# Optimization experiments

Measured on AMD Instinct MI355X. Metric: run time of the kernel, lower is better.

The kernel has to match this reference:

```python
import jax, jax.numpy as jnp
import numpy as np

ALPHA = 32.0 ** 2
HEADS = 8
DIM_HEAD = 64
EPS = 1e-5


def _leaky(x):
    return jnp.where(x >= 0, x, 0.1 * x)


def _cpb_bias(fmap_size, w0, b0, w1, b1, w2, b2):
    # continuous position bias: MLP over signed-log relative coords -> [h, n, n]
    pos = jnp.arange(fmap_size)
    gi, gj = jnp.meshgrid(pos, pos, indexing='ij')
    grid = jnp.stack([gi, gj], axis=-1).reshape(-1, 2)  # [n, 2]
    rel = grid[:, None, :] - grid[None, :, :]           # [n, n, 2]
    rel = jnp.sign(rel) * jnp.log(jnp.abs(rel) + 1.0)
    h = _leaky(jnp.einsum('ijc,dc->ijd', rel.astype(jnp.float32), w0) + b0)
    h = _leaky(jnp.einsum('ijc,dc->ijd', h, w1) + b1)
    h = jnp.einsum('ijc,hc->ijh', h, w2) + b2           # [n, n, heads]
    return jnp.transpose(h, (2, 0, 1))                  # [heads, n, n]


def _stable_softmax(t, alpha=ALPHA):
    t = t / alpha
    t = t - jax.lax.stop_gradient(jnp.max(t, axis=-1, keepdims=True))
    return jax.nn.softmax(t * alpha, axis=-1)


def setup_inputs() -> dict:
    key = jax.random.key(0)
    ks = jax.random.split(key, 9)
    B, C, H, W = 8, 512, 32, 32
    inner = HEADS * DIM_HEAD
    s = 0.05
    return {
        'x': jax.random.normal(ks[0], (B, C, H, W), jnp.float32),
        'gamma': jnp.ones((1, C, 1, 1), jnp.float32),
        'w_qkv': jax.random.normal(ks[1], (inner * 3, C), jnp.float32) * s,
        'w_out': jax.random.normal(ks[2], (C, inner), jnp.float32) * s,
        'cpb_w0': jax.random.normal(ks[3], (128, 2), jnp.float32) * s,
        'cpb_b0': jax.random.normal(ks[4], (128,), jnp.float32) * s,
        'cpb_w1': jax.random.normal(ks[5], (128, 128), jnp.float32) * s,
        'cpb_b1': jax.random.normal(ks[6], (128,), jnp.float32) * s,
        'cpb_w2': jax.random.normal(ks[7], (HEADS, 128), jnp.float32) * s,
        'cpb_b2': jax.random.normal(ks[8], (HEADS,), jnp.float32) * s,
    }


def reference(x, gamma, w_qkv, w_out, cpb_w0, cpb_b0, cpb_w1, cpb_b1, cpb_w2, cpb_b2):
    B, C, H, W = x.shape
    n = H * W
    scale = DIM_HEAD ** -0.5
    residual = x

    # LayerNormChan: normalize over channel dim with biased variance
    mean = jnp.mean(x, axis=1, keepdims=True)
    var = jnp.var(x, axis=1, keepdims=True)
    xn = (x - mean) / jnp.sqrt(var + EPS) * gamma

    # 1x1 conv qkv projection as matmul over channels
    xf = xn.reshape(B, C, n)                              # [B, C, n]
    qkv = jnp.einsum('oc,bcn->bon', w_qkv, xf)            # [B, 3*inner, n]
    q, k, v = jnp.split(qkv, 3, axis=1)
    rs = lambda t: t.reshape(B, HEADS, DIM_HEAD, n)
    q, k, v = rs(q), rs(k), rs(v)

    sim = jnp.einsum('bhdi,bhdj->bhij', q, k) * scale     # [B, h, n, n]
    bias = _cpb_bias(H, cpb_w0, cpb_b0, cpb_w1, cpb_b1, cpb_w2, cpb_b2)
    sim = sim + bias[None]

    attn = _stable_softmax(sim)
    out = jnp.einsum('bhij,bhdj->bhdi', attn, v)          # [B, h, d, n]
    out = out.reshape(B, HEADS * DIM_HEAD, n)
    out = jnp.einsum('oc,bcn->bon', w_out, out).reshape(B, C, H, W)
    return out + residual
```

## Files before the change

kernel.cpp:

```cpp
#include <hip/hip_runtime.h>
#include <hip/hip_bf16.h>

#define CCH   512
#define BATCH 8
#define NPOS  1024
#define MQKV  1536
#define EPS   1e-5f
#define LOG2E 1.4426950408889634f

typedef __attribute__((ext_vector_type(4))) float f32x4;
typedef __attribute__((ext_vector_type(8))) __bf16 bf16x8;
typedef __attribute__((ext_vector_type(8))) unsigned short u16x8;
typedef __attribute__((ext_vector_type(4))) unsigned short u16x4;

__device__ inline unsigned short f2bf(float f) {
  __hip_bfloat16 h = __float2bfloat16(f);
  return __builtin_bit_cast(unsigned short, h);
}
__device__ inline float bf2f(unsigned short u) {
  return __bfloat162float(__builtin_bit_cast(__hip_bfloat16, u));
}

__device__ inline int sw(int row, int col) { return row * 64 + (col ^ ((row & 7) << 3)); }

__device__ inline void gload16(const void* g, void* l) {
  __builtin_amdgcn_global_load_lds((const __attribute__((address_space(1))) void*)g,
                                   (__attribute__((address_space(3))) void*)l, 16, 0, 0);
}

__global__ __launch_bounds__(256) void setup_kernel(
    const float* __restrict__ wq, const float* __restrict__ wo,
    unsigned short* __restrict__ wqb, unsigned short* __restrict__ wob,
    const float* __restrict__ x, const float* __restrict__ gamma,
    unsigned short* __restrict__ xnT) {
  __shared__ float red[4][32][2];
  __shared__ float gsh[512];
  __shared__ unsigned short obuf[32 * 520];
  int bid = blockIdx.x, tid = threadIdx.x;

  if (bid < 3072) {
    int i = bid * 256 + tid;
    if (i < MQKV * CCH) {
      float v = wq[i];
      if (i < 512 * CCH) v *= 0.125f * LOG2E;
      wqb[i] = f2bf(v);
    }
    if (i < CCH * CCH) wob[i] = f2bf(wo[i]);
  } else {
    int blk = bid - 3072;
    int b = blk >> 5, p0 = (blk & 31) * 32;
    int pl = tid & 31, wv = tid >> 6, cg = tid >> 5;
    gsh[tid] = gamma[tid];
    gsh[tid + 256] = gamma[tid + 256];
    const float* xp = x + (size_t)b * CCH * NPOS + p0 + pl;
    float vals[64];
    float s1 = 0.f, s2 = 0.f;
    #pragma unroll
    for (int j = 0; j < 64; ++j) {
      float v = xp[(size_t)(cg + 8 * j) * NPOS];
      vals[j] = v; s1 += v; s2 += v * v;
    }
    s1 += __shfl_xor(s1, 32, 64); s2 += __shfl_xor(s2, 32, 64);
    if ((tid & 63) < 32) { red[wv][pl][0] = s1; red[wv][pl][1] = s2; }
    __syncthreads();
    float t1 = 0.f, t2 = 0.f;
    #pragma unroll
    for (int w2i = 0; w2i < 4; ++w2i) { t1 += red[w2i][pl][0]; t2 += red[w2i][pl][1]; }
    float mean = t1 * (1.f / 512.f);
    float var = t2 * (1.f / 512.f) - mean * mean;
    float rstd = rsqrtf(var + EPS);
    #pragma unroll
    for (int j = 0; j < 64; ++j) {
      int c = cg + 8 * j;
      obuf[pl * 520 + c] = f2bf((vals[j] - mean) * rstd * gsh[c]);
    }
    __syncthreads();
    unsigned short* orow = xnT + ((size_t)b * NPOS + p0) * 512;
    #pragma unroll
    for (int i = 0; i < 8; ++i) {
      int c2 = tid + i * 256;
      int pp = c2 >> 6, ch = c2 & 63;
      *(u16x8*)&orow[(size_t)pp * 512 + ch * 8] = *(const u16x8*)&obuf[pp * 520 + ch * 8];
    }
  }
}

__global__ __launch_bounds__(256) void cpb_kernel(
    const float* __restrict__ w0, const float* __restrict__ b0,
    const float* __restrict__ w1, const float* __restrict__ b1,
    const float* __restrict__ w2, const float* __restrict__ b2,
    float* __restrict__ table) {
  __shared__ float w1s[128 * 129];
  __shared__ float w2s[8 * 128];
  __shared__ float sh1[2][128];
  __shared__ float sh2[2][128];
  int tid = threadIdx.x;
  #pragma unroll
  for (int i = 0; i < 64; ++i) {
    int idx = i * 256 + tid;
    w1s[(idx >> 7) * 129 + (idx & 127)] = w1[idx];
  }
  #pragma unroll
  for (int i = 0; i < 4; ++i) {
    int idx = i * 256 + tid;
    w2s[idx] = w2[idx];
  }
  int sub = tid >> 7, t = tid & 127;
  float w00 = w0[t * 2 + 0], w01 = w0[t * 2 + 1], bb0 = b0[t], bb1 = b1[t];
  int hh = t >> 4, k16 = t & 15;
  float b2h = b2[hh];
  __syncthreads();

  #pragma unroll 1
  for (int pass = 0; pass < 8; ++pass) {
    int d0 = (blockIdx.x * 8 + pass) * 2 + sub;
    bool ok = d0 < 3969;
    int d0c = ok ? d0 : 0;
    int dy = d0c / 63 - 31, dx = d0c % 63 - 31;
    float r0 = (dy > 0 ? 1.f : (dy < 0 ? -1.f : 0.f)) * logf(fabsf((float)dy) + 1.f);
    float r1 = (dx > 0 ? 1.f : (dx < 0 ? -1.f : 0.f)) * logf(fabsf((float)dx) + 1.f);
    float h0 = r0 * w00 + r1 * w01 + bb0;
    sh1[sub][t] = (h0 >= 0.f) ? h0 : 0.1f * h0;
    __syncthreads();
    float a = bb1;
    #pragma unroll 8
    for (int c = 0; c < 128; ++c) a += sh1[sub][c] * w1s[t * 129 + c];
    sh2[sub][t] = (a >= 0.f) ? a : 0.1f * a;
    __syncthreads();
    float o = 0.f;
    #pragma unroll
    for (int c = 0; c < 8; ++c) o += sh2[sub][k16 * 8 + c] * w2s[hh * 128 + k16 * 8 + c];
    #pragma unroll
    for (int mm = 1; mm < 16; mm <<= 1) o += __shfl_xor(o, mm, 64);
    if (k16 == 0 && ok) table[hh * 3969 + d0] = (o + b2h) * LOG2E;
    __syncthreads();
  }
}

__global__ void bias_expand(const float* __restrict__ table, unsigned short* __restrict__ biasP) {
  int idx = blockIdx.x * 256 + threadIdx.x;
  int h = idx >> 20;
  int i = (idx >> 10) & 1023;
  int blk = (idx >> 6) & 15;
  int q = idx & 63;
  int l16 = q >> 2, jt = q & 3;
  int j = blk * 64 + jt * 16 + l16;
  int dy = (i >> 5) - (j >> 5) + 31;
  int dx = (i & 31) - (j & 31) + 31;
  biasP[idx] = f2bf(table[h * 3969 + dy * 63 + dx]);
}

__global__ __launch_bounds__(256) void gemm_qkv(const unsigned short* __restrict__ Ag,
                                                const unsigned short* __restrict__ Bg,
                                                unsigned short* __restrict__ qT,
                                                unsigned short* __restrict__ kT,
                                                unsigned short* __restrict__ vB) {
  __shared__ unsigned short smem[2 * 128 * 64];
  unsigned short* As = smem;
  unsigned short* Bs = smem + 128 * 64;
  int tid = threadIdx.x;
  int by = blockIdx.y;
  int m0 = by * 128, nn0 = blockIdx.x * 128;
  int wave = tid >> 6, lane = tid & 63;
  int wm = wave >> 1, wn = wave & 1;
  int l16 = lane & 15, lh = lane >> 4;
  int rsub = lane >> 3, csub = lane & 7;
  int scsw = (csub ^ rsub) * 8;
  f32x4 acc[4][4];
  #pragma unroll
  for (int it = 0; it < 4; ++it)
    #pragma unroll
    for (int jt = 0; jt < 4; ++jt) acc[it][jt] = (f32x4){0.f, 0.f, 0.f, 0.f};

  for (int k0 = 0; k0 < 512; k0 += 64) {
    #pragma unroll
    for (int i = 0; i < 4; ++i) {
      int grp = wave * 4 + i;
      int row = grp * 8 + rsub;
      gload16(&Ag[(size_t)(m0 + row) * 512 + k0 + scsw], &As[grp * 512]);
      gload16(&Bg[(size_t)(nn0 + row) * 512 + k0 + scsw], &Bs[grp * 512]);
    }
    __syncthreads();
    #pragma unroll
    for (int ks = 0; ks < 2; ++ks) {
      int koff = ks * 32 + lh * 8;
      bf16x8 a[4], b[4];
      #pragma unroll
      for (int it = 0; it < 4; ++it) a[it] = *(const bf16x8*)&As[sw(wm * 64 + it * 16 + l16, koff)];
      #pragma unroll
      for (int jt = 0; jt < 4; ++jt) b[jt] = *(const bf16x8*)&Bs[sw(wn * 64 + jt * 16 + l16, koff)];
      #pragma unroll
      for (int it = 0; it < 4; ++it)
        #pragma unroll
        for (int jt = 0; jt < 4; ++jt)
          acc[it][jt] = __builtin_amdgcn_mfma_f32_16x16x32_bf16(a[it], b[jt], acc[it][jt], 0, 0, 0);
    }
    __syncthreads();
  }

  int sel = by >> 2;
  int hh0 = (by & 3) * 2;
  int bb = nn0 >> 10, p0 = nn0 & 1023;
  unsigned short* Cs = smem;
  if (sel < 2) {
    #pragma unroll
    for (int it = 0; it < 4; ++it)
      #pragma unroll
      for (int jt = 0; jt < 4; ++jt) {
        int nnl = wn * 64 + jt * 16 + l16;
        int mb = wm * 64 + it * 16 + lh * 4;
        #pragma unroll
        for (int r = 0; r < 4; ++r)
          Cs[nnl * 128 + ((mb + r) ^ ((nnl & 7) << 4))] = f2bf(acc[it][jt][r]);
      }
    __syncthreads();
    unsigned short* dst = (sel == 0) ? qT : kT;
    #pragma unroll
    for (int i = 0; i < 8; ++i) {
      int c = tid + i * 256;
      int hl = c >> 10, p = (c >> 3) & 127, ch = c & 7;
      int mb = hl * 64 + ch * 8;
      u16x8 val = *(u16x8*)&Cs[p * 128 + (mb ^ ((p & 7) << 4))];
      int bh = bb * 8 + hh0 + hl;
      *(u16x8*)&dst[((size_t)bh * 1024 + p0 + p) * 64 + ch * 8] = val;
    }
  } else {
    #pragma unroll
    for (int it = 0; it < 4; ++it)
      #pragma unroll
      for (int jt = 0; jt < 4; ++jt) {
        int nnl = wn * 64 + jt * 16 + l16;
        int mb = wm * 64 + it * 16 + lh * 4;
        #pragma unroll
        for (int r = 0; r < 4; ++r)
          Cs[(mb + r) * 128 + (nnl ^ (((mb + r) & 7) << 4))] = f2bf(acc[it][jt][r]);
      }
    __syncthreads();
    #pragma unroll
    for (int i = 0; i < 8; ++i) {
      int c = tid + i * 256;
      int mloc = c >> 4, ch = c & 15;
      u16x8 val = *(u16x8*)&Cs[mloc * 128 + ((ch * 8) ^ ((mloc & 7) << 4))];
      int d = mloc & 63, hl = mloc >> 6;
      int bh = bb * 8 + hh0 + hl;
      *(u16x8*)&vB[((size_t)bh * 64 + d) * 1024 + p0 + ch * 8] = val;
    }
  }
}

__global__ __launch_bounds__(256) void gemm_out(const unsigned short* __restrict__ Ag,
                                                const unsigned short* __restrict__ Bg,
                                                const float* __restrict__ xres,
                                                float* __restrict__ yout) {
  __shared__ unsigned short As[64 * 64];
  __shared__ unsigned short Bs[128 * 64];
  int tid = threadIdx.x;
  int m0 = blockIdx.y * 64, nn0 = blockIdx.x * 128;
  int wave = tid >> 6, lane = tid & 63;
  int wm = wave >> 1, wn = wave & 1;
  int l16 = lane & 15, lh = lane >> 4;
  int rsub = lane >> 3, csub = lane & 7;
  int scsw = (csub ^ rsub) * 8;
  f32x4 acc[2][4];
  #pragma unroll
  for (int it = 0; it < 2; ++it)
    #pragma unroll
    for (int jt = 0; jt < 4; ++jt) acc[it][jt] = (f32x4){0.f, 0.f, 0.f, 0.f};

  for (int k0 = 0; k0 < 512; k0 += 64) {
    #pragma unroll
    for (int i = 0; i < 2; ++i) {
      int grp = wave * 2 + i;
      gload16(&Ag[(size_t)(m0 + grp * 8 + rsub) * 512 + k0 + scsw], &As[grp * 512]);
    }
    #pragma unroll
    for (int i = 0; i < 4; ++i) {
      int grp = wave * 4 + i;
      gload16(&Bg[(size_t)(nn0 + grp * 8 + rsub) * 512 + k0 + scsw], &Bs[grp * 512]);
    }
    __syncthreads();
    #pragma unroll
    for (int ks = 0; ks < 2; ++ks) {
      int koff = ks * 32 + lh * 8;
      bf16x8 a[2], b[4];
      #pragma unroll
      for (int it = 0; it < 2; ++it) a[it] = *(const bf16x8*)&As[sw(wm * 32 + it * 16 + l16, koff)];
      #pragma unroll
      for (int jt = 0; jt < 4; ++jt) b[jt] = *(const bf16x8*)&Bs[sw(wn * 64 + jt * 16 + l16, koff)];
      #pragma unroll
      for (int it = 0; it < 2; ++it)
        #pragma unroll
        for (int jt = 0; jt < 4; ++jt)
          acc[it][jt] = __builtin_amdgcn_mfma_f32_16x16x32_bf16(a[it], b[jt], acc[it][jt], 0, 0, 0);
    }
    __syncthreads();
  }

  #pragma unroll
  for (int it = 0; it < 2; ++it) {
    int mbase = m0 + wm * 32 + it * 16 + lh * 4;
    #pragma unroll
    for (int jt = 0; jt < 4; ++jt) {
      int nn = nn0 + wn * 64 + jt * 16 + l16;
      int bb = nn >> 10, p = nn & 1023;
      #pragma unroll
      for (int r = 0; r < 4; ++r) {
        size_t addr = ((size_t)bb * 512 + mbase + r) * 1024 + p;
        yout[addr] = acc[it][jt][r] + xres[addr];
      }
    }
  }
}

__global__ __launch_bounds__(512) void attn_kernel(const unsigned short* __restrict__ qT,
                                                   const unsigned short* __restrict__ kT,
                                                   const unsigned short* __restrict__ vB,
                                                   const unsigned short* __restrict__ biasP,
                                                   unsigned short* __restrict__ attnout) {
  __shared__ unsigned short Kbuf[2][64 * 64];
  __shared__ unsigned short Vbuf[2][64 * 64];
  __shared__ unsigned short Ps[8][16 * 64];
  int tid = threadIdx.x;
  int bh = blockIdx.x;
  int i0 = blockIdx.y * 128;
  int hh = bh & 7, bb = bh >> 3;
  int w = tid >> 6, lane = tid & 63, l16 = lane & 15, lh = lane >> 4;
  int rsub = lane >> 3, csub = lane & 7;
  int scsw = (csub ^ rsub) * 8;

  const unsigned short* kbase = kT + (size_t)bh * NPOS * 64;
  const unsigned short* vbase = vB + (size_t)bh * 64 * NPOS;
  const unsigned short* bptr  = biasP + ((size_t)hh * 1024 + i0 + w * 16) * 1024 + l16 * 4;

  int qrow = i0 + w * 16 + l16;
  const unsigned short* qb = qT + ((size_t)bh * NPOS + qrow) * 64 + lh * 8;
  bf16x8 qreg[2];
  qreg[0] = *(const bf16x8*)&qb[0];
  qreg[1] = *(const bf16x8*)&qb[32];

  f32x4 o[5];
  #pragma unroll
  for (int dt = 0; dt < 5; ++dt) o[dt] = (f32x4){0.f, 0.f, 0.f, 0.f};

  bf16x8 ones;
  {
    u16x8 tmp = {0x3F80, 0x3F80, 0x3F80, 0x3F80, 0x3F80, 0x3F80, 0x3F80, 0x3F80};
    ones = __builtin_bit_cast(bf16x8, tmp);
  }

  #define STAGE(Kd, Vd, jj) do {                                                        \
    gload16(&kbase[(size_t)((jj) + w * 8 + rsub) * 64 + scsw], &(Kd)[w * 512]);         \
    gload16(&vbase[(size_t)(w * 8 + rsub) * 1024 + (jj) + scsw], &(Vd)[w * 512]);       \
  } while (0)

  STAGE(Kbuf[0], Vbuf[0], 0);
  __syncthreads();

  #pragma unroll 1
  for (int t = 0; t < 16; ++t) {
    int j0 = t * 64;
    if (t < 15) STAGE(Kbuf[(t + 1) & 1], Vbuf[(t + 1) & 1], j0 + 64);

    const unsigned short* Ks = Kbuf[t & 1];
    const unsigned short* Vs = Vbuf[t & 1];

    u16x4 bv4[4];
    #pragma unroll
    for (int r = 0; r < 4; ++r) bv4[r] = *(const u16x4*)&bptr[(lh * 4 + r) * 1024 + j0];

    f32x4 s[4];
    #pragma unroll
    for (int jt = 0; jt < 4; ++jt) s[jt] = (f32x4){0.f, 0.f, 0.f, 0.f};
    #pragma unroll
    for (int ks = 0; ks < 2; ++ks) {
      int koff = ks * 32 + lh * 8;
      #pragma unroll
      for (int jt = 0; jt < 4; ++jt) {
        bf16x8 bk = *(const bf16x8*)&Ks[sw(jt * 16 + l16, koff)];
        s[jt] = __builtin_amdgcn_mfma_f32_16x16x32_bf16(qreg[ks], bk, s[jt], 0, 0, 0);
      }
    }

    #pragma unroll
    for (int r = 0; r < 4; ++r) {
      int rloc = lh * 4 + r;
      #pragma unroll
      for (int jt = 0; jt < 4; ++jt) {
        float pv = __builtin_amdgcn_exp2f(s[jt][r] + bf2f(bv4[r][jt]));
        Ps[w][sw(rloc, jt * 16 + l16)] = f2bf(pv);
      }
    }

    #pragma unroll
    for (int js = 0; js < 2; ++js) {
      int koff = js * 32 + lh * 8;
      bf16x8 pa = *(const bf16x8*)&Ps[w][sw(l16, koff)];
      #pragma unroll
      for (int dt = 0; dt < 4; ++dt) {
        bf16x8 vb = *(const bf16x8*)&Vs[sw(dt * 16 + l16, koff)];
        o[dt] = __builtin_amdgcn_mfma_f32_16x16x32_bf16(pa, vb, o[dt], 0, 0, 0);
      }
      o[4] = __builtin_amdgcn_mfma_f32_16x16x32_bf16(pa, ones, o[4], 0, 0, 0);
    }

    __syncthreads();
  }

  #pragma unroll
  for (int r = 0; r < 4; ++r) {
    float inv = 1.f / o[4][r];
    int gi = i0 + w * 16 + lh * 4 + r;
    #pragma unroll
    for (int dt = 0; dt < 4; ++dt)
      attnout[((size_t)bb * 1024 + gi) * 512 + hh * 64 + dt * 16 + l16] = f2bf(o[dt][r] * inv);
  }
}

extern "C" void kernel_launch(void* const* d_in, const int* in_sizes, int n_in,
                              void* d_out, int out_size, void* d_ws, size_t ws_size,
                              hipStream_t stream) {
  const float* x     = (const float*)d_in[0];
  const float* gamma = (const float*)d_in[1];
  const float* w_qkv = (const float*)d_in[2];
  const float* w_out = (const float*)d_in[3];
  const float* cw0   = (const float*)d_in[4];
  const float* cb0   = (const float*)d_in[5];
  const float* cw1   = (const float*)d_in[6];
  const float* cb1   = (const float*)d_in[7];
  const float* cw2   = (const float*)d_in[8];
  const float* cb2   = (const float*)d_in[9];
  float* out = (float*)d_out;

  char* ws = (char*)d_ws;
  unsigned short* xnT   = (unsigned short*)(ws + 0);
  unsigned short* wqb   = (unsigned short*)(ws + 8388608);
  unsigned short* wob   = (unsigned short*)(ws + 9961472);
  unsigned short* qT    = (unsigned short*)(ws + 10485760);
  unsigned short* kT    = (unsigned short*)(ws + 18874368);
  unsigned short* vB    = (unsigned short*)(ws + 27262976);
  float*          table = (float*)(ws + 35651584);
  unsigned short* biasP = (unsigned short*)(ws + 35782656);
  unsigned short* aout  = (unsigned short*)(ws + 52559872);

  cpb_kernel<<<256, 256, 0, stream>>>(cw0, cb0, cw1, cb1, cw2, cb2, table);
  setup_kernel<<<3328, 256, 0, stream>>>(w_qkv, w_out, wqb, wob, x, gamma, xnT);
  bias_expand<<<32768, 256, 0, stream>>>(table, biasP);
  gemm_qkv<<<dim3(64, 12), 256, 0, stream>>>(wqb, xnT, qT, kT, vB);
  attn_kernel<<<dim3(64, 8), 512, 0, stream>>>(qT, kT, vB, biasP, aout);
  gemm_out<<<dim3(64, 8), 256, 0, stream>>>(wob, aout, x, out);
}
```

Measured before the change: 116.1 us.

## Double-buffer GEMM K-tiles, vectorize bias expansion, raise MFMA wave priority

Both GEMMs now stage 32-wide K tiles into double-buffered LDS, with a new 32-column swizzle, so global-to-LDS loads for the next tile overlap MFMA work on the current one. bias_expand now writes eight bf16 values per thread with a single vector store and launches one eighth as many blocks. s_setprio is raised around the MFMA blocks in the GEMMs and the attention kernel so those waves are favoured by the scheduler. The smaller K step doubles the number of loop iterations and barriers, and the new swizzle must stay consistent between the staged loads and the fragment reads.

```diff
diff --git a/kernel.cpp b/kernel.cpp
--- a/kernel.cpp
+++ b/kernel.cpp
@@ -22,6 +22,9 @@
 }
 
 __device__ inline int sw(int row, int col) { return row * 64 + (col ^ ((row & 7) << 3)); }
+__device__ inline int sw32(int row, int lh) {
+  return row * 32 + ((lh ^ ((row ^ (row >> 2)) & 3)) << 3);
+}
 
 __device__ inline void gload16(const void* g, void* l) {
   __builtin_amdgcn_global_load_lds((const __attribute__((address_space(1))) void*)g,
@@ -138,16 +141,23 @@
 }
 
 __global__ void bias_expand(const float* __restrict__ table, unsigned short* __restrict__ biasP) {
-  int idx = blockIdx.x * 256 + threadIdx.x;
-  int h = idx >> 20;
-  int i = (idx >> 10) & 1023;
-  int blk = (idx >> 6) & 15;
-  int q = idx & 63;
-  int l16 = q >> 2, jt = q & 3;
-  int j = blk * 64 + jt * 16 + l16;
-  int dy = (i >> 5) - (j >> 5) + 31;
-  int dx = (i & 31) - (j & 31) + 31;
-  biasP[idx] = f2bf(table[h * 3969 + dy * 63 + dx]);
+  int base = (blockIdx.x * 256 + threadIdx.x) * 8;
+  int h = base >> 20;
+  int i = (base >> 10) & 1023;
+  int blk = (base >> 6) & 15;
+  int q0 = base & 63;
+  int ib = i >> 5, il = i & 31;
+  u16x8 outv;
+  #pragma unroll
+  for (int e = 0; e < 8; ++e) {
+    int q = q0 + e;
+    int l16 = q >> 2, jt = q & 3;
+    int j = blk * 64 + jt * 16 + l16;
+    int dy = ib - (j >> 5) + 31;
+    int dx = il - (j & 31) + 31;
+    outv[e] = f2bf(table[h * 3969 + dy * 63 + dx]);
+  }
+  *(u16x8*)&biasP[base] = outv;
 }
 
 __global__ __launch_bounds__(256) void gemm_qkv(const unsigned short* __restrict__ Ag,
@@ -155,46 +165,51 @@
                                                 unsigned short* __restrict__ qT,
                                                 unsigned short* __restrict__ kT,
                                                 unsigned short* __restrict__ vB) {
-  __shared__ unsigned short smem[2 * 128 * 64];
-  unsigned short* As = smem;
-  unsigned short* Bs = smem + 128 * 64;
+  __shared__ unsigned short smem[16384];
   int tid = threadIdx.x;
   int by = blockIdx.y;
   int m0 = by * 128, nn0 = blockIdx.x * 128;
   int wave = tid >> 6, lane = tid & 63;
   int wm = wave >> 1, wn = wave & 1;
   int l16 = lane & 15, lh = lane >> 4;
-  int rsub = lane >> 3, csub = lane & 7;
-  int scsw = (csub ^ rsub) * 8;
+  int r4 = lane >> 2, c4 = lane & 3;
+  int csw = ((c4 ^ (r4 & 3) ^ ((lane >> 4) & 3))) << 3;
   f32x4 acc[4][4];
   #pragma unroll
   for (int it = 0; it < 4; ++it)
     #pragma unroll
     for (int jt = 0; jt < 4; ++jt) acc[it][jt] = (f32x4){0.f, 0.f, 0.f, 0.f};
 
-  for (int k0 = 0; k0 < 512; k0 += 64) {
-    #pragma unroll
-    for (int i = 0; i < 4; ++i) {
-      int grp = wave * 4 + i;
-      int row = grp * 8 + rsub;
-      gload16(&Ag[(size_t)(m0 + row) * 512 + k0 + scsw], &As[grp * 512]);
-      gload16(&Bg[(size_t)(nn0 + row) * 512 + k0 + scsw], &Bs[grp * 512]);
-    }
-    __syncthreads();
-    #pragma unroll
-    for (int ks = 0; ks < 2; ++ks) {
-      int koff = ks * 32 + lh * 8;
-      bf16x8 a[4], b[4];
-      #pragma unroll
-      for (int it = 0; it < 4; ++it) a[it] = *(const bf16x8*)&As[sw(wm * 64 + it * 16 + l16, koff)];
-      #pragma unroll
-      for (int jt = 0; jt < 4; ++jt) b[jt] = *(const bf16x8*)&Bs[sw(wn * 64 + jt * 16 + l16, koff)];
-      #pragma unroll
-      for (int it = 0; it < 4; ++it)
-        #pragma unroll
-        for (int jt = 0; jt < 4; ++jt)
-          acc[it][jt] = __builtin_amdgcn_mfma_f32_16x16x32_bf16(a[it], b[jt], acc[it][jt], 0, 0, 0);
-    }
+  #define GSTAGE(bsel, k0) do {                                                               \
+    _Pragma("unroll")                                                                         \
+    for (int i_ = 0; i_ < 2; ++i_) {                                                          \
+      int grp_ = wave * 2 + i_;                                                               \
+      int row_ = grp_ * 16 + r4;                                                              \
+      gload16(&Ag[(size_t)(m0 + row_) * 512 + (k0) + csw], smem + (bsel) * 4096 + grp_ * 512);\
+      gload16(&Bg[(size_t)(nn0 + row_) * 512 + (k0) + csw],                                   \
+              smem + 8192 + (bsel) * 4096 + grp_ * 512);                                      \
+    }                                                                                         \
+  } while (0)
+
+  GSTAGE(0, 0);
+  __syncthreads();
+  #pragma unroll 1
+  for (int k = 0; k < 16; ++k) {
+    if (k < 15) GSTAGE((k + 1) & 1, (k + 1) * 32);
+    const unsigned short* As = smem + (k & 1) * 4096;
+    const unsigned short* Bs = smem + 8192 + (k & 1) * 4096;
+    bf16x8 a[4], b[4];
+    #pragma unroll
+    for (int it = 0; it < 4; ++it) a[it] = *(const bf16x8*)&As[sw32(wm * 64 + it * 16 + l16, lh)];
+    #pragma unroll
+    for (int jt = 0; jt < 4; ++jt) b[jt] = *(const bf16x8*)&Bs[sw32(wn * 64 + jt * 16 + l16, lh)];
+    __builtin_amdgcn_s_setprio(1);
+    #pragma unroll
+    for (int it = 0; it < 4; ++it)
+      #pragma unroll
+      for (int jt = 0; jt < 4; ++jt)
+        acc[it][jt] = __builtin_amdgcn_mfma_f32_16x16x32_bf16(a[it], b[jt], acc[it][jt], 0, 0, 0);
+    __builtin_amdgcn_s_setprio(0);
     __syncthreads();
   }
 
@@ -252,47 +267,54 @@
                                                 const unsigned short* __restrict__ Bg,
                                                 const float* __restrict__ xres,
                                                 float* __restrict__ yout) {
-  __shared__ unsigned short As[64 * 64];
-  __shared__ unsigned short Bs[128 * 64];
+  __shared__ unsigned short smem[12288];
   int tid = threadIdx.x;
   int m0 = blockIdx.y * 64, nn0 = blockIdx.x * 128;
   int wave = tid >> 6, lane = tid & 63;
   int wm = wave >> 1, wn = wave & 1;
   int l16 = lane & 15, lh = lane >> 4;
-  int rsub = lane >> 3, csub = lane & 7;
-  int scsw = (csub ^ rsub) * 8;
+  int r4 = lane >> 2, c4 = lane & 3;
+  int csw = ((c4 ^ (r4 & 3) ^ ((lane >> 4) & 3))) << 3;
   f32x4 acc[2][4];
   #pragma unroll
   for (int it = 0; it < 2; ++it)
     #pragma unroll
     for (int jt = 0; jt < 4; ++jt) acc[it][jt] = (f32x4){0.f, 0.f, 0.f, 0.f};
 
-  for (int k0 = 0; k0 < 512; k0 += 64) {
-    #pragma unroll
-    for (int i = 0; i < 2; ++i) {
-      int grp = wave * 2 + i;
-      gload16(&Ag[(size_t)(m0 + grp * 8 + rsub) * 512 + k0 + scsw], &As[grp * 512]);
-    }
-    #pragma unroll
-    for (int i = 0; i < 4; ++i) {
-      int grp = wave * 4 + i;
-      gload16(&Bg[(size_t)(nn0 + grp * 8 + rsub) * 512 + k0 + scsw], &Bs[grp * 512]);
-    }
-    __syncthreads();
-    #pragma unroll
-    for (int ks = 0; ks < 2; ++ks) {
-      int koff = ks * 32 + lh * 8;
-      bf16x8 a[2], b[4];
-      #pragma unroll
-      for (int it = 0; it < 2; ++it) a[it] = *(const bf16x8*)&As[sw(wm * 32 + it * 16 + l16, koff)];
-      #pragma unroll
-      for (int jt = 0; jt < 4; ++jt) b[jt] = *(const bf16x8*)&Bs[sw(wn * 64 + jt * 16 + l16, koff)];
-      #pragma unroll
-      for (int it = 0; it < 2; ++it)
-        #pragma unroll
-        for (int jt = 0; jt < 4; ++jt)
-          acc[it][jt] = __builtin_amdgcn_mfma_f32_16x16x32_bf16(a[it], b[jt], acc[it][jt], 0, 0, 0);
-    }
+  #define OSTAGE(bsel, k0) do {                                                               \
+    {                                                                                         \
+      int row_ = wave * 16 + r4;                                                              \
+      gload16(&Ag[(size_t)(m0 + row_) * 512 + (k0) + csw],                                    \
+              smem + (bsel) * 2048 + wave * 512);                                             \
+    }                                                                                         \
+    _Pragma("unroll")                                                                         \
+    for (int i_ = 0; i_ < 2; ++i_) {                                                          \
+      int grp_ = wave * 2 + i_;                                                               \
+      int row_ = grp_ * 16 + r4;                                                              \
+      gload16(&Bg[(size_t)(nn0 + row_) * 512 + (k0) + csw],                                   \
+              smem + 4096 + (bsel) * 4096 + grp_ * 512);                                      \
+    }                                                                                         \
+  } while (0)
+
+  OSTAGE(0, 0);
+  __syncthreads();
+  #pragma unroll 1
+  for (int k = 0; k < 16; ++k) {
+    if (k < 15) OSTAGE((k + 1) & 1, (k + 1) * 32);
+    const unsigned short* As = smem + (k & 1) * 2048;
+    const unsigned short* Bs = smem + 4096 + (k & 1) * 4096;
+    bf16x8 a[2], b[4];
+    #pragma unroll
+    for (int it = 0; it < 2; ++it) a[it] = *(const bf16x8*)&As[sw32(wm * 32 + it * 16 + l16, lh)];
+    #pragma unroll
+    for (int jt = 0; jt < 4; ++jt) b[jt] = *(const bf16x8*)&Bs[sw32(wn * 64 + jt * 16 + l16, lh)];
+    __builtin_amdgcn_s_setprio(1);
+    #pragma unroll
+    for (int it = 0; it < 2; ++it)
+      #pragma unroll
+      for (int jt = 0; jt < 4; ++jt)
+        acc[it][jt] = __builtin_amdgcn_mfma_f32_16x16x32_bf16(a[it], b[jt], acc[it][jt], 0, 0, 0);
+    __builtin_amdgcn_s_setprio(0);
     __syncthreads();
   }
 
@@ -371,6 +393,7 @@
     f32x4 s[4];
     #pragma unroll
     for (int jt = 0; jt < 4; ++jt) s[jt] = (f32x4){0.f, 0.f, 0.f, 0.f};
+    __builtin_amdgcn_s_setprio(1);
     #pragma unroll
     for (int ks = 0; ks < 2; ++ks) {
       int koff = ks * 32 + lh * 8;
@@ -380,6 +403,7 @@
         s[jt] = __builtin_amdgcn_mfma_f32_16x16x32_bf16(qreg[ks], bk, s[jt], 0, 0, 0);
       }
     }
+    __builtin_amdgcn_s_setprio(0);
 
     #pragma unroll
     for (int r = 0; r < 4; ++r) {
@@ -391,6 +415,7 @@
       }
     }
 
+    __builtin_amdgcn_s_setprio(1);
     #pragma unroll
     for (int js = 0; js < 2; ++js) {
       int koff = js * 32 + lh * 8;
@@ -402,6 +427,7 @@
       }
       o[4] = __builtin_amdgcn_mfma_f32_16x16x32_bf16(pa, ones, o[4], 0, 0, 0);
     }
+    __builtin_amdgcn_s_setprio(0);
 
     __syncthreads();
   }
@@ -444,7 +470,7 @@
 
   cpb_kernel<<<256, 256, 0, stream>>>(cw0, cb0, cw1, cb1, cw2, cb2, table);
   setup_kernel<<<3328, 256, 0, stream>>>(w_qkv, w_out, wqb, wob, x, gamma, xnT);
-  bias_expand<<<32768, 256, 0, stream>>>(table, biasP);
+  bias_expand<<<4096, 256, 0, stream>>>(table, biasP);
   gemm_qkv<<<dim3(64, 12), 256, 0, stream>>>(wqb, xnT, qT, kT, vB);
   attn_kernel<<<dim3(64, 8), 512, 0, stream>>>(qT, kT, vB, biasP, aout);
   gemm_out<<<dim3(64, 8), 256, 0, stream>>>(wob, aout, x, out);
```

Result: faster. 110.2 us (-5.1%).
